# Kernel optimization log

Measured on AMD Instinct MI355X. Metric: run time of the kernel, lower is better.

Reference implementation:

```python
import jax, jax.numpy as jnp
import numpy as np

NUM_ROUTING = 3

def squash(v, axis=-1):
    # scale = s2 / (1 + s2) / sqrt(s2), same as the TF source (no epsilon)
    s2 = jnp.sum(jnp.square(v), axis=axis, keepdims=True)
    scale = s2 / (1.0 + s2) / jnp.sqrt(s2)
    return scale * v


def setup_inputs() -> dict:
    key = jax.random.key(0)
    k1, k2 = jax.random.split(key)
    B, I, D = 128, 1152, 8   # batch, input_num_capsule, input_dim_vector
    C, E = 32, 16            # num_capsule, dim_vector
    x = jax.random.normal(k1, (B, I, D), dtype=jnp.float32)
    W = jax.random.normal(k2, (I, C, D, E), dtype=jnp.float32) * 0.05
    return {"x": x, "W": W}


def reference(x, W):
    # x: [B, I, D]; W: [I, C, D, E]
    B, I, D = x.shape
    C, E = W.shape[1], W.shape[3]
    # inputs_hat: u_hat[b,i,c,e] = sum_d x[b,i,d] * W[i,c,d,e]
    # (the TF code serializes this over batch via tf.scan; math is a batched GEMM)
    u_hat = jnp.einsum('bid,icde->bice', x, W)  # [B, I, C, E]
    # routing logits; TF bias has shape [1, I, C, 1, 1] and becomes per-batch
    # [B, I, C, 1, 1] after the first += (broadcast). We track [*, I, C].
    b = jnp.zeros((1, I, C), dtype=x.dtype)
    outputs = None
    for i in range(NUM_ROUTING):
        c = jax.nn.softmax(b, axis=2)[..., None]           # [*, I, C, 1]
        s = jnp.sum(c * u_hat, axis=1, keepdims=True)      # [B, 1, C, E]
        outputs = squash(s)                                # [B, 1, C, E]
        if i != NUM_ROUTING - 1:
            b = b + jnp.sum(u_hat * outputs, axis=-1)      # [B, I, C]
    return outputs.reshape(B, C, E)
```

## Files before the change

### kernel.cpp

```cpp
#include <hip/hip_runtime.h>
#include <hip/hip_fp16.h>
#include <math.h>

#define BATCH 128
#define NI    1152
#define ND    8
#define NC    32
#define NE    16
#define NROUT 3

#define ISPLIT     48
#define GTILES     6
#define BT         8
#define NB         2
#define RT_THREADS 256
#define CROW       68
#define TLDSW      (NC * CROW)
#define SQ_THREADS 256
#define PREP_TPB   2

typedef _Float16 h2 __attribute__((ext_vector_type(2)));
typedef unsigned int uint;

__device__ __forceinline__ h2 cvt_pk(float a, float b) {
    auto r = __builtin_amdgcn_cvt_pkrtz(a, b);
    union { decltype(r) i; h2 o; } u; u.i = r; return u.o;
}
__device__ __forceinline__ uint h2u(h2 v) { union { h2 h; uint u; } x; x.h = v; return x.u; }
__device__ __forceinline__ h2 u2h(uint v) { union { uint u; h2 h; } x; x.u = v; return x.h; }

#if __has_builtin(__builtin_amdgcn_fdot2)
#define FDOT2(a, b, c) __builtin_amdgcn_fdot2((a), (b), (c), false)
#else
__device__ __forceinline__ float FDOT2(h2 a, h2 b, float c) {
    return c + (float)a.x * (float)b.x + (float)a.y * (float)b.y;
}
#endif

template<int CTRL>
__device__ __forceinline__ float dpp_add(float v) {
    int t = __builtin_amdgcn_update_dpp(0, __float_as_int(v), CTRL, 0xF, 0xF, true);
    return v + __int_as_float(t);
}

__device__ __forceinline__ float xor32_sum(float v) {
#if __has_builtin(__builtin_amdgcn_permlane32_swap)
    auto r = __builtin_amdgcn_permlane32_swap(__float_as_int(v), __float_as_int(v), false, false);
    return __int_as_float(r[0]) + __int_as_float(r[1]);
#else
    return v + __shfl_xor(v, 32);
#endif
}
__device__ __forceinline__ float xor16_sum(float v) {
#if __has_builtin(__builtin_amdgcn_permlane16_swap)
    auto r = __builtin_amdgcn_permlane16_swap(__float_as_int(v), __float_as_int(v), false, false);
    return __int_as_float(r[0]) + __int_as_float(r[1]);
#else
    int s = __builtin_amdgcn_ds_swizzle(__float_as_int(v), 0x401F);
    return v + __int_as_float(s);
#endif
}

__device__ __forceinline__ float sum_over_e8(float v) {
    v = dpp_add<0xB1>(v);
    v = dpp_add<0x4E>(v);
    v = dpp_add<0x141>(v);
    return v;
}

__global__ __launch_bounds__(RT_THREADS)
void prep_kernel(const float* __restrict__ W, uint* __restrict__ W_hp)
{
    __shared__ float ls[PREP_TPB][NC * 132];

    const int tid = threadIdx.x;
    const size_t i0 = (size_t)blockIdx.x * PREP_TPB;

    const float4* src = (const float4*)(W + i0 * (NC * ND * NE));
#pragma unroll
    for (int t = 0; t < PREP_TPB; ++t) {
#pragma unroll
        for (int r = 0; r < 4; ++r) {
            int g = tid + r * RT_THREADS;
            float4 v = src[t * 1024 + g];
            *(float4*)&ls[t][(g >> 5) * 132 + (g & 31) * 4] = v;
        }
    }
    __syncthreads();

#pragma unroll
    for (int t = 0; t < PREP_TPB; ++t) {
#pragma unroll
        for (int r = 0; r < 2; ++r) {
            int g = tid + r * RT_THREADS;
            int c = g >> 4, e = g & 15;
            const float* p = &ls[t][c * 132 + e];
            uint4 o;
            o.x = h2u(cvt_pk(p[0],  p[16]));
            o.y = h2u(cvt_pk(p[32], p[48]));
            o.z = h2u(cvt_pk(p[64], p[80]));
            o.w = h2u(cvt_pk(p[96], p[112]));
            *(uint4*)&W_hp[(i0 + t) * TLDSW + c * CROW + e * 4] = o;
        }
    }
}

__global__ __launch_bounds__(RT_THREADS)
void route_iter_kernel(const float* __restrict__ x, const uint* __restrict__ W_hp,
                       const float* __restrict__ o_sum, __half* __restrict__ s_part,
                       int iter)
{
    constexpr int ICHUNK_T = NI / ISPLIT;
    constexpr int NGROUP_T = ICHUNK_T / GTILES;
    static_assert(NGROUP_T * GTILES == ICHUNK_T, "group split");

    __shared__ uint Wh[GTILES * TLDSW];

    const int tid = threadIdx.x;
    const int c   = tid & 31;
    const int eh  = (tid >> 5) & 1;
    int wid;
    asm("v_mov_b32 %0, %1" : "=v"(wid) : "v"(tid >> 6));
    const int ic  = blockIdx.x;
    const int bt  = blockIdx.y;
    const int i0  = ic * ICHUNK_T;
    const int b0  = bt * BT + wid * NB;
    const int e0  = eh * 8;

    float o_reg[NB][8];
    if (iter > 0) {
#pragma unroll
        for (int j = 0; j < NB; ++j) {
            const float4* op = (const float4*)(o_sum + ((size_t)(b0 + j) * NC + c) * NE + e0);
            float4 a = op[0], b = op[1];
            o_reg[j][0] = a.x; o_reg[j][1] = a.y; o_reg[j][2] = a.z; o_reg[j][3] = a.w;
            o_reg[j][4] = b.x; o_reg[j][5] = b.y; o_reg[j][6] = b.z; o_reg[j][7] = b.w;
        }
    }

    float s_acc[NB][8];
#pragma unroll
    for (int j = 0; j < NB; ++j)
#pragma unroll
        for (int e = 0; e < 8; ++e) s_acc[j][e] = 0.f;

    const float* xp[NB];
    float4 xnA[NB][2], xnB[NB][2];
#pragma unroll
    for (int j = 0; j < NB; ++j) {
        xp[j] = x + ((size_t)(b0 + j) * NI + i0) * ND;
        xnA[j][0] = *(const float4*)xp[j];
        xnA[j][1] = *(const float4*)(xp[j] + 4);
    }

    const uint* wbase = &Wh[c * CROW + e0 * 4];

    auto body = [&](const float4 (&XC)[NB][2], float4 (&XN)[NB][2], int t, int II) {
        if (II + 1 < ICHUNK_T) {
#pragma unroll
            for (int j = 0; j < NB; ++j) {
                xp[j] += ND;
                XN[j][0] = *(const float4*)xp[j];
                XN[j][1] = *(const float4*)(xp[j] + 4);
            }
        }

        h2 xq[NB][4];
#pragma unroll
        for (int j = 0; j < NB; ++j) {
            xq[j][0] = cvt_pk(XC[j][0].x, XC[j][0].y);
            xq[j][1] = cvt_pk(XC[j][0].z, XC[j][0].w);
            xq[j][2] = cvt_pk(XC[j][1].x, XC[j][1].y);
            xq[j][3] = cvt_pk(XC[j][1].z, XC[j][1].w);
        }

        const uint* wr = wbase + t * TLDSW;
        float uh[NB][8];
#pragma unroll
        for (int er = 0; er < 8; ++er) {
            uint4 wv = *(const uint4*)(wr + er * 4);
            h2 w0 = u2h(wv.x), w1 = u2h(wv.y), w2 = u2h(wv.z), w3 = u2h(wv.w);
#pragma unroll
            for (int j = 0; j < NB; ++j) {
                float acc = 0.f;
                acc = FDOT2(xq[j][0], w0, acc);
                acc = FDOT2(xq[j][1], w1, acc);
                acc = FDOT2(xq[j][2], w2, acc);
                acc = FDOT2(xq[j][3], w3, acc);
                uh[j][er] = acc;
            }
        }

        if (iter > 0) {
#pragma unroll
            for (int j = 0; j < NB; ++j) {
                float lp = 0.f;
#pragma unroll
                for (int e = 0; e < 8; ++e) lp = fmaf(uh[j][e], o_reg[j][e], lp);
                lp = xor32_sum(lp);
                float el = __expf(lp);
                float v = dpp_add<0x140>(dpp_add<0x141>(
                          dpp_add<0x4E>(dpp_add<0xB1>(el))));
                float den = xor16_sum(v);
                float wgt = el * __builtin_amdgcn_rcpf(den);
#pragma unroll
                for (int e = 0; e < 8; ++e) s_acc[j][e] = fmaf(wgt, uh[j][e], s_acc[j][e]);
            }
        } else {
            const float wgt = 1.f / 32.f;
#pragma unroll
            for (int j = 0; j < NB; ++j)
#pragma unroll
                for (int e = 0; e < 8; ++e) s_acc[j][e] = fmaf(wgt, uh[j][e], s_acc[j][e]);
        }
    };

#pragma unroll
    for (int g = 0; g < NGROUP_T; ++g) {
        if (g) __syncthreads();
        {
            constexpr int TOT4 = GTILES * TLDSW / 4;
            const uint4* src = (const uint4*)(W_hp + (size_t)(i0 + g * GTILES) * TLDSW);
            uint4* dst = (uint4*)Wh;
#pragma unroll
            for (int k = 0; k < (TOT4 + RT_THREADS - 1) / RT_THREADS; ++k) {
                int idx = tid + k * RT_THREADS;
                if (TOT4 % RT_THREADS == 0 || idx < TOT4)
                    dst[idx] = src[idx];
            }
        }
        __syncthreads();

#pragma unroll
        for (int tp = 0; tp < GTILES; ++tp) {
            int II = g * GTILES + tp;
            if ((II & 1) == 0) body(xnA, xnB, tp, II);
            else               body(xnB, xnA, tp, II);
        }
    }

#pragma unroll
    for (int j = 0; j < NB; ++j) {
        __half* base = s_part + (((size_t)ic * BATCH + (b0 + j)) * NC + c) * NE + e0;
        union { __half2 h2v[4]; uint4 u; } pk;
#pragma unroll
        for (int q = 0; q < 4; ++q)
            pk.h2v[q] = __floats2half2_rn(s_acc[j][2*q], s_acc[j][2*q+1]);
        *(uint4*)base = pk.u;
    }
}

__global__ __launch_bounds__(SQ_THREADS)
void squash_kernel(const __half* __restrict__ s_part, float* __restrict__ o_sum,
                   float* __restrict__ out, int iter)
{
    const int base2 = (blockIdx.x * SQ_THREADS + threadIdx.x) * 2;

    float a0 = 0.f, a1 = 0.f;
#pragma unroll 8
    for (int k = 0; k < ISPLIT; ++k) {
        __half2 v = *(const __half2*)(s_part + (size_t)k * (BATCH * NC * NE) + base2);
        a0 += __low2float(v);
        a1 += __high2float(v);
    }

    float q = sum_over_e8(a0 * a0 + a1 * a1);
    float scale = sqrtf(q) / (1.f + q);
    float o0 = scale * a0, o1 = scale * a1;

    if (iter == NROUT - 1) {
        *(float2*)(out + base2) = make_float2(o0, o1);
    } else if (iter == 0) {
        *(float2*)(o_sum + base2) = make_float2(o0, o1);
    } else {
        float2 prev = *(float2*)(o_sum + base2);
        *(float2*)(o_sum + base2) = make_float2(prev.x + o0, prev.y + o1);
    }
}

extern "C" void kernel_launch(void* const* d_in, const int* in_sizes, int n_in,
                              void* d_out, int out_size, void* d_ws, size_t ws_size,
                              hipStream_t stream) {
    const float* x = (const float*)d_in[0];
    const float* W = (const float*)d_in[1];
    float* out = (float*)d_out;

    const size_t whp_words = (size_t)NI * TLDSW;
    const size_t slice_h   = (size_t)BATCH * NC * NE;

    uint*   W_hp   = (uint*)d_ws;
    __half* s_part = (__half*)(W_hp + whp_words);
    float*  o_sum  = (float*)(s_part + (size_t)ISPLIT * slice_h);

    prep_kernel<<<NI / PREP_TPB, RT_THREADS, 0, stream>>>(W, W_hp);

    for (int it = 0; it < NROUT; ++it) {
        route_iter_kernel<<<dim3(ISPLIT, BATCH / BT), RT_THREADS, 0, stream>>>(
            x, W_hp, o_sum, s_part, it);
        squash_kernel<<<(BATCH * NC * NE) / (SQ_THREADS * 2), SQ_THREADS, 0, stream>>>(
            s_part, o_sum, out, it);
    }
}
```

Baseline: 105.0 us.

## Double-buffer W tiles in LDS with register prefetch of next group

Replaces the single LDS buffer of 6 tiles, which was loaded synchronously before each compute group, with two 3-tile buffers. The next group's W is prefetched from global memory into registers, stored to the alternate LDS buffer after the current group's compute, and then guarded by a single custom barrier. The goal is to hide global-load latency behind the FMA/dot work and drop one barrier per group. The cost is higher register pressure from holding the prefetch in registers, plus a raw s_barrier that depends on a correct lgkmcnt wait.

```diff
diff --git a/kernel.cpp b/kernel.cpp
--- a/kernel.cpp
+++ b/kernel.cpp
@@ -10,7 +10,7 @@
 #define NROUT 3
 
 #define ISPLIT     48
-#define GTILES     6
+#define GT         3
 #define BT         8
 #define NB         2
 #define RT_THREADS 256
@@ -66,6 +66,12 @@
     v = dpp_add<0x4E>(v);
     v = dpp_add<0x141>(v);
     return v;
+}
+
+__device__ __forceinline__ void lds_barrier() {
+    asm volatile("s_waitcnt lgkmcnt(0)" ::: "memory");
+    __builtin_amdgcn_s_barrier();
+    __builtin_amdgcn_sched_barrier(0);
 }
 
 __global__ __launch_bounds__(RT_THREADS)
@@ -111,10 +117,12 @@
                        int iter)
 {
     constexpr int ICHUNK_T = NI / ISPLIT;
-    constexpr int NGROUP_T = ICHUNK_T / GTILES;
-    static_assert(NGROUP_T * GTILES == ICHUNK_T, "group split");
-
-    __shared__ uint Wh[GTILES * TLDSW];
+    constexpr int NG       = ICHUNK_T / GT;
+    constexpr int TOT4     = GT * TLDSW / 4;
+    constexpr int LPT      = (TOT4 + RT_THREADS - 1) / RT_THREADS;
+    static_assert(NG * GT == ICHUNK_T, "group split");
+
+    __shared__ uint Wh[2][GT * TLDSW];
 
     const int tid = threadIdx.x;
     const int c   = tid & 31;
@@ -153,9 +161,10 @@
         xnA[j][1] = *(const float4*)(xp[j] + 4);
     }
 
-    const uint* wbase = &Wh[c * CROW + e0 * 4];
-
-    auto body = [&](const float4 (&XC)[NB][2], float4 (&XN)[NB][2], int t, int II) {
+    const uint* wbase = &Wh[0][c * CROW + e0 * 4];
+
+    auto body = [&](const float4 (&XC)[NB][2], float4 (&XN)[NB][2],
+                    int buf, int tp, int II) {
         if (II + 1 < ICHUNK_T) {
 #pragma unroll
             for (int j = 0; j < NB; ++j) {
@@ -174,7 +183,7 @@
             xq[j][3] = cvt_pk(XC[j][1].z, XC[j][1].w);
         }
 
-        const uint* wr = wbase + t * TLDSW;
+        const uint* wr = wbase + (buf * GT + tp) * TLDSW;
         float uh[NB][8];
 #pragma unroll
         for (int er = 0; er < 8; ++er) {
@@ -215,27 +224,49 @@
         }
     };
 
-#pragma unroll
-    for (int g = 0; g < NGROUP_T; ++g) {
-        if (g) __syncthreads();
-        {
-            constexpr int TOT4 = GTILES * TLDSW / 4;
-            const uint4* src = (const uint4*)(W_hp + (size_t)(i0 + g * GTILES) * TLDSW);
-            uint4* dst = (uint4*)Wh;
-#pragma unroll
-            for (int k = 0; k < (TOT4 + RT_THREADS - 1) / RT_THREADS; ++k) {
+    const uint4* gsrc = (const uint4*)(W_hp + (size_t)i0 * TLDSW);
+    uint4 pr[LPT];
+
+#pragma unroll
+    for (int k = 0; k < LPT; ++k) {
+        int idx = tid + k * RT_THREADS;
+        if (idx < TOT4) pr[k] = gsrc[idx];
+    }
+#pragma unroll
+    for (int k = 0; k < LPT; ++k) {
+        int idx = tid + k * RT_THREADS;
+        if (idx < TOT4) ((uint4*)Wh[0])[idx] = pr[k];
+    }
+#pragma unroll
+    for (int k = 0; k < LPT; ++k) {
+        int idx = tid + k * RT_THREADS;
+        if (idx < TOT4) pr[k] = gsrc[TOT4 + idx];
+    }
+    lds_barrier();
+
+#pragma unroll
+    for (int g = 0; g < NG; ++g) {
+        const int buf = g & 1;
+#pragma unroll
+        for (int tp = 0; tp < GT; ++tp) {
+            int II = g * GT + tp;
+            if ((II & 1) == 0) body(xnA, xnB, buf, tp, II);
+            else               body(xnB, xnA, buf, tp, II);
+        }
+        if (g + 1 < NG) {
+#pragma unroll
+            for (int k = 0; k < LPT; ++k) {
                 int idx = tid + k * RT_THREADS;
-                if (TOT4 % RT_THREADS == 0 || idx < TOT4)
-                    dst[idx] = src[idx];
-            }
-        }
-        __syncthreads();
-
-#pragma unroll
-        for (int tp = 0; tp < GTILES; ++tp) {
-            int II = g * GTILES + tp;
-            if ((II & 1) == 0) body(xnA, xnB, tp, II);
-            else               body(xnB, xnA, tp, II);
+                if (idx < TOT4) ((uint4*)Wh[(g + 1) & 1])[idx] = pr[k];
+            }
+            if (g + 2 < NG) {
+#pragma unroll
+                for (int k = 0; k < LPT; ++k) {
+                    int idx = tid + k * RT_THREADS;
+                    if (idx < TOT4) pr[k] = gsrc[(size_t)(g + 2) * TOT4 + idx];
+                }
+            }
+            lds_barrier();
         }
     }
 
```

Result: slower. 185.3 us (+76.5%).
